# Optimization experiments

Hardware: AMD Instinct MI355X
Metric: run time of the kernel (lower is better)

The kernel has to match this reference:

```python
import jax, jax.numpy as jnp
import numpy as np

N = 131072
N_DIM = 128
NUM_LAYERS = 8
N_MID = NUM_LAYERS - 2  # middle (n_dim -> n_dim) layers


def _sigmoid_layer(h, u_un, w_un, log_a, b):
    # h: [N, in]; u_un: [out, in]; w_un: [out, out]; log_a, b: [out, 1]
    a = jnp.exp(log_a)                      # [out, 1]
    u = jax.nn.softmax(u_un, axis=1)        # row-softmax, matches Softmax(dim=1)
    w = jax.nn.softmax(w_un, axis=1)
    inner = h @ (a * u).T + b[:, 0]         # [N, out]
    return jax.nn.sigmoid(inner) @ w.T      # [N, out]


def setup_inputs() -> dict:
    key = jax.random.key(0)
    ks = jax.random.split(key, 24)
    d = N_DIM
    inp = {
        "x": jax.random.normal(ks[0], (N,), jnp.float32),
        "fy0": jax.random.normal(ks[1], (N,), jnp.float32),
        # first layer (in=2, out=d)
        "u0": jax.random.normal(ks[2], (d, 2), jnp.float32),
        "w0": jax.random.normal(ks[3], (d, d), jnp.float32),
        "la0": jax.random.normal(ks[4], (d, 1), jnp.float32),
        "b0": jax.random.normal(ks[5], (d, 1), jnp.float32),
        # middle layers stacked (in=d, out=d)
        "uM": jax.random.normal(ks[6], (N_MID, d, d), jnp.float32),
        "wM": jax.random.normal(ks[7], (N_MID, d, d), jnp.float32),
        "laM": jax.random.normal(ks[8], (N_MID, d, 1), jnp.float32),
        "bM": jax.random.normal(ks[9], (N_MID, d, 1), jnp.float32),
        # last layer (in=d, out=1)
        "uL": jax.random.normal(ks[10], (1, d), jnp.float32),
        "wL": jax.random.normal(ks[11], (1, 1), jnp.float32),
        "laL": jax.random.normal(ks[12], (1, 1), jnp.float32),
        "bL": jax.random.normal(ks[13], (1, 1), jnp.float32),
        # MLP 1 -> 50 -> 50 -> 1
        "W1": jax.random.normal(ks[14], (50, 1), jnp.float32) * 0.2,
        "b1": jax.random.normal(ks[15], (50,), jnp.float32) * 0.2,
        "W2": jax.random.normal(ks[16], (50, 50), jnp.float32) * 0.1,
        "b2": jax.random.normal(ks[17], (50,), jnp.float32) * 0.1,
        "W3": jax.random.normal(ks[18], (1, 50), jnp.float32) * 0.1,
        "b3": jax.random.normal(ks[19], (1,), jnp.float32) * 0.1,
    }
    return inp


def reference(x, fy0, u0, w0, la0, b0, uM, wM, laM, bM, uL, wL, laL, bL,
              W1, b1, W2, b2, W3, b3):
    # MLP feature net on fy0: [N,1] -> [N,1]
    h = jax.nn.relu(fy0[:, None] @ W1.T + b1)
    h = jax.nn.relu(h @ W2.T + b2)
    theta = h @ W3.T + b3                          # [N, 1]
    mono = jnp.concatenate([x[:, None], theta], 1)  # [N, 2]

    mono = _sigmoid_layer(mono, u0, w0, la0, b0)    # [N, d]

    def step(carry, p):
        u_un, w_un, log_a, b = p
        return _sigmoid_layer(carry, u_un, w_un, log_a, b), None

    mono, _ = jax.lax.scan(step, mono, (uM, wM, laM, bM))
    out = _sigmoid_layer(mono, uL, wL, laL, bL)     # [N, 1]
    return out[:, :, None]                          # [N, 1, 1] matches torch
```

## Files before the change

kernel.cpp:

```cpp
#include <hip/hip_runtime.h>
#include <cstdint>

typedef __attribute__((ext_vector_type(8))) _Float16 half8;
typedef __attribute__((ext_vector_type(2))) _Float16 half2v;
typedef __attribute__((ext_vector_type(16))) float f32x16;
typedef __attribute__((ext_vector_type(4))) float f4;

#define LOG2E 1.44269504088896340f

__device__ __forceinline__ float fast_exp(float x) { return __builtin_amdgcn_exp2f(LOG2E * x); }
__device__ __forceinline__ float sigmoidf(float v) {
    return __builtin_amdgcn_rcpf(1.f + __builtin_amdgcn_exp2f(-LOG2E * v));
}
__device__ __forceinline__ unsigned pk2(float a, float b) {
    half2v h = { (_Float16)a, (_Float16)b };
    return __builtin_bit_cast(unsigned, h);
}
__device__ __forceinline__ void swapl(unsigned& a, unsigned& b) {
    asm volatile("v_permlane32_swap_b32 %0, %1" : "+v"(a), "+v"(b));
}
__device__ __forceinline__ void swaplf(float& a, float& b) {
    asm volatile("v_permlane32_swap_b32 %0, %1" : "+v"(a), "+v"(b));
}
union BU { unsigned u[4]; half8 h; };

constexpr int A0X = 0, A0T = 128, B0O = 256, BMO = 384, VLO = 1152,
              W1P = 1280, B1P = 1344, B2P = 1408, W3P = 1472, ULSF = 1536, CN = 1664;

constexpr int GOFF  = 0;
constexpr int W2HI  = 6 * 65536;
constexpr int W2LO  = W2HI + 8192;
constexpr int CGOFF = W2LO + 8192;
constexpr int WFOFF = CGOFF + 8192;
constexpr int AFOFF = WFOFF + 7 * 65536;

__global__ void prep1_kernel(const float* __restrict__ u0, const float* __restrict__ w0,
                             const float* __restrict__ la0, const float* __restrict__ b0,
                             const float* __restrict__ uM, const float* __restrict__ wM,
                             const float* __restrict__ laM, const float* __restrict__ bM,
                             const float* __restrict__ uL, const float* __restrict__ laL,
                             const float* __restrict__ W1, const float* __restrict__ b1,
                             const float* __restrict__ W2, const float* __restrict__ b2,
                             const float* __restrict__ W3,
                             float* __restrict__ Wf, float* __restrict__ Af,
                             _Float16* __restrict__ W2hi, _Float16* __restrict__ W2lo,
                             float* __restrict__ CgF)
{
    const int b = blockIdx.x, lane = threadIdx.x;
    if (b < 1664) {
        const int m = b >> 7, r = b & 127;
        const float* src;
        float scale = 1.f;
        float* dst;
        if (m == 0) {
            src = w0 + r * 128;
            dst = Wf + r * 128;
        } else if (m & 1) {
            int l = (m - 1) >> 1;
            src = uM + (l * 128 + r) * 128;
            scale = fast_exp(laM[l * 128 + r]);
            dst = Af + l * 16384 + r * 128;
        } else {
            int l = (m - 2) >> 1;
            src = wM + (l * 128 + r) * 128;
            dst = Wf + (l + 1) * 16384 + r * 128;
        }
        float v0 = src[lane], v1 = src[lane + 64];
        float mx = fmaxf(v0, v1);
#pragma unroll
        for (int o = 32; o; o >>= 1) mx = fmaxf(mx, __shfl_xor(mx, o));
        float e0 = fast_exp(v0 - mx), e1 = fast_exp(v1 - mx);
        float ssum = e0 + e1;
#pragma unroll
        for (int o = 32; o; o >>= 1) ssum += __shfl_xor(ssum, o);
        float inv = scale / ssum;
        dst[lane]      = e0 * inv;
        dst[lane + 64] = e1 * inv;
    } else if (b == 1664) {
        for (int j = lane; j < 128; j += 64) {
            float q0 = u0[2 * j], q1 = u0[2 * j + 1];
            float mx = fmaxf(q0, q1);
            float e0 = fast_exp(q0 - mx), e1 = fast_exp(q1 - mx);
            float a = fast_exp(la0[j]) / (e0 + e1);
            CgF[A0X + j] = a * e0;
            CgF[A0T + j] = a * e1;
            CgF[B0O + j] = b0[j];
        }
        CgF[W1P + lane] = (lane < 50) ? W1[lane] : 0.f;
        CgF[B1P + lane] = (lane < 50) ? b1[lane] : 0.f;
        CgF[B2P + lane] = (lane < 50) ? b2[lane] : 0.f;
        CgF[W3P + lane] = (lane < 50) ? W3[lane] : 0.f;
        for (int i = lane; i < 768; i += 64) CgF[BMO + i] = bM[i];
    } else if (b == 1665) {
        float v0 = uL[lane], v1 = uL[lane + 64];
        float mx = fmaxf(v0, v1);
#pragma unroll
        for (int o = 32; o; o >>= 1) mx = fmaxf(mx, __shfl_xor(mx, o));
        float e0 = fast_exp(v0 - mx), e1 = fast_exp(v1 - mx);
        float ssum = e0 + e1;
#pragma unroll
        for (int o = 32; o; o >>= 1) ssum += __shfl_xor(ssum, o);
        float aL = fast_exp(laL[0]) / ssum;
        CgF[ULSF + lane]      = e0 * aL;
        CgF[ULSF + 64 + lane] = e1 * aL;
    } else {
        for (int i = lane; i < 4096; i += 64) {
            int r = i >> 6, c = i & 63;
            float v = (r < 50 && c < 50) ? W2[r * 50 + c] : 0.f;
            _Float16 h = (_Float16)v;
            W2hi[i] = h;
            W2lo[i] = (_Float16)(v - (float)h);
        }
    }
}

__global__ void prep2_kernel(const float* __restrict__ Wf, const float* __restrict__ Af,
                             char* __restrict__ G, float* __restrict__ CgF)
{
    const int b = blockIdx.x, lane = threadIdx.x;
    if (b < 768) {
        const int l = b >> 7, i = b & 127;
        const float* Arow = Af + l * 16384 + i * 128;
        const float* W = Wf + l * 16384;
        float m0 = 0.f, m1 = 0.f;
        for (int k = 0; k < 128; ++k) {
            float a = Arow[k];
            m0 += a * W[k * 128 + lane];
            m1 += a * W[k * 128 + lane + 64];
        }
        char* basehi = G + l * 65536 + i * 256;
        char* baselo = basehi + 32768;
        const int sw = (i & 7) << 4;
        _Float16 h0 = (_Float16)m0, h1 = (_Float16)m1;
        *(_Float16*)(basehi + ((2 * lane) ^ sw))        = h0;
        *(_Float16*)(basehi + ((2 * (lane + 64)) ^ sw)) = h1;
        *(_Float16*)(baselo + ((2 * lane) ^ sw))        = (_Float16)(m0 - (float)h0);
        *(_Float16*)(baselo + ((2 * (lane + 64)) ^ sw)) = (_Float16)(m1 - (float)h1);
    } else {
        const float* W6 = Wf + 6 * 16384;
        float m0 = 0.f, m1 = 0.f;
        for (int i = 0; i < 128; ++i) {
            float u = CgF[ULSF + i];
            m0 += u * W6[i * 128 + lane];
            m1 += u * W6[i * 128 + lane + 64];
        }
        CgF[VLO + lane]      = m0;
        CgF[VLO + 64 + lane] = m1;
    }
}


__device__ __forceinline__ void stage64(char* ls, const char* gs, int tid) {
#pragma unroll
    for (int i = 0; i < 8; ++i)
        __builtin_amdgcn_global_load_lds(
            (const __attribute__((address_space(1))) unsigned*)(uintptr_t)(gs + tid * 16 + i * 8192),
            (__attribute__((address_space(3))) unsigned*)(uintptr_t)(ls + tid * 16 + i * 8192),
            16, 0, 0);
}

__device__ __forceinline__ void epi_nt(const f32x16& a0, const f32x16& a1,
                                       half8& o00, half8& o01, half8& o10, half8& o11,
                                       const float* __restrict__ biasNT, int hi)
{
    f4 bv0 = *(const f4*)(biasNT + 4 * hi);
    f4 bv1 = *(const f4*)(biasNT + 8 + 4 * hi);
    f4 bv2 = *(const f4*)(biasNT + 16 + 4 * hi);
    f4 bv3 = *(const f4*)(biasNT + 24 + 4 * hi);
#pragma unroll
    for (int bt = 0; bt < 2; ++bt) {
        const f32x16& A = bt ? a1 : a0;
        unsigned p00 = pk2(sigmoidf(A[0] + bv0[0]),  sigmoidf(A[1] + bv0[1]));
        unsigned p01 = pk2(sigmoidf(A[2] + bv0[2]),  sigmoidf(A[3] + bv0[3]));
        unsigned p10 = pk2(sigmoidf(A[4] + bv1[0]),  sigmoidf(A[5] + bv1[1]));
        unsigned p11 = pk2(sigmoidf(A[6] + bv1[2]),  sigmoidf(A[7] + bv1[3]));
        unsigned p20 = pk2(sigmoidf(A[8] + bv2[0]),  sigmoidf(A[9] + bv2[1]));
        unsigned p21 = pk2(sigmoidf(A[10] + bv2[2]), sigmoidf(A[11] + bv2[3]));
        unsigned p30 = pk2(sigmoidf(A[12] + bv3[0]), sigmoidf(A[13] + bv3[1]));
        unsigned p31 = pk2(sigmoidf(A[14] + bv3[2]), sigmoidf(A[15] + bv3[3]));
        swapl(p00, p10); swapl(p01, p11);
        swapl(p20, p30); swapl(p21, p31);
        BU u0; u0.u[0] = p00; u0.u[1] = p01; u0.u[2] = p10; u0.u[3] = p11;
        BU u1; u1.u[0] = p20; u1.u[1] = p21; u1.u[2] = p30; u1.u[3] = p31;
        if (bt == 0) { o00 = u0.h; o01 = u1.h; }
        else         { o10 = u0.h; o11 = u1.h; }
    }
}

__device__ __forceinline__ void do_layer(const char* buf,
                                         const half8 (&Bin)[2][8], half8 (&Bout)[2][8],
                                         const float* __restrict__ biasL,
                                         int l31, int hi)
{
    const int sw = (l31 & 7) << 4;
#pragma unroll
    for (int nt = 0; nt < 4; ++nt) {
        f32x16 a0 = {}, a1 = {};
        const char* rhi = buf + (nt * 32 + l31) * 256;
        const char* rlo = rhi + 32768;
#pragma unroll
        for (int ks = 0; ks < 8; ++ks) {
            const int off = (ks * 32 + hi * 16) ^ sw;
            half8 Ah = *(const half8*)(rhi + off);
            half8 Al = *(const half8*)(rlo + off);
            a0 = __builtin_amdgcn_mfma_f32_32x32x16_f16(Ah, Bin[0][ks], a0, 0, 0, 0);
            a1 = __builtin_amdgcn_mfma_f32_32x32x16_f16(Ah, Bin[1][ks], a1, 0, 0, 0);
            a0 = __builtin_amdgcn_mfma_f32_32x32x16_f16(Al, Bin[0][ks], a0, 0, 0, 0);
            a1 = __builtin_amdgcn_mfma_f32_32x32x16_f16(Al, Bin[1][ks], a1, 0, 0, 0);
        }
        epi_nt(a0, a1, Bout[0][2 * nt], Bout[0][2 * nt + 1],
               Bout[1][2 * nt], Bout[1][2 * nt + 1], biasL + 32 * nt, hi);
    }
}

__global__ __launch_bounds__(512, 2)
void mono_main(const float* __restrict__ x, const float* __restrict__ fy0,
               const char* __restrict__ G,
               const _Float16* __restrict__ W2hi, const _Float16* __restrict__ W2lo,
               const float* __restrict__ CgF, const float* __restrict__ b3g,
               const float* __restrict__ bLg, float* __restrict__ out)
{
    extern __shared__ __align__(16) char sm[];
    char* buf0 = sm;
    char* buf1 = sm + 65536;

    const int tid = threadIdx.x;
    const int lane = tid & 63, wave = tid >> 6;
    const int l31 = lane & 31, hi = lane >> 5;
    const int row0 = blockIdx.x * 512 + wave * 64;

    stage64(buf0, G, tid);
    const float b3s = b3g[0], bLs = bLg[0];

    float fy[2] = { fy0[row0 + l31], fy0[row0 + 32 + l31] };
    half8 Bm[2][4];
#pragma unroll
    for (int ks = 0; ks < 4; ++ks) {
        f4 w1a = *(const f4*)(CgF + W1P + 16 * ks + 8 * hi);
        f4 w1b = *(const f4*)(CgF + W1P + 16 * ks + 8 * hi + 4);
        f4 b1a = *(const f4*)(CgF + B1P + 16 * ks + 8 * hi);
        f4 b1b = *(const f4*)(CgF + B1P + 16 * ks + 8 * hi + 4);
#pragma unroll
        for (int bt = 0; bt < 2; ++bt) {
            BU u;
            u.u[0] = pk2(fmaxf(fy[bt] * w1a[0] + b1a[0], 0.f), fmaxf(fy[bt] * w1a[1] + b1a[1], 0.f));
            u.u[1] = pk2(fmaxf(fy[bt] * w1a[2] + b1a[2], 0.f), fmaxf(fy[bt] * w1a[3] + b1a[3], 0.f));
            u.u[2] = pk2(fmaxf(fy[bt] * w1b[0] + b1b[0], 0.f), fmaxf(fy[bt] * w1b[1] + b1b[1], 0.f));
            u.u[3] = pk2(fmaxf(fy[bt] * w1b[2] + b1b[2], 0.f), fmaxf(fy[bt] * w1b[3] + b1b[3], 0.f));
            Bm[bt][ks] = u.h;
        }
    }

    f32x16 a00 = {}, a01 = {}, a10 = {}, a11 = {};
#pragma unroll
    for (int nt = 0; nt < 2; ++nt)
#pragma unroll
        for (int ks = 0; ks < 4; ++ks) {
            half8 Ah = *(const half8*)(W2hi + (nt * 32 + l31) * 64 + ks * 16 + hi * 8);
            half8 Al = *(const half8*)(W2lo + (nt * 32 + l31) * 64 + ks * 16 + hi * 8);
            if (nt == 0) {
                a00 = __builtin_amdgcn_mfma_f32_32x32x16_f16(Ah, Bm[0][ks], a00, 0, 0, 0);
                a10 = __builtin_amdgcn_mfma_f32_32x32x16_f16(Ah, Bm[1][ks], a10, 0, 0, 0);
                a00 = __builtin_amdgcn_mfma_f32_32x32x16_f16(Al, Bm[0][ks], a00, 0, 0, 0);
                a10 = __builtin_amdgcn_mfma_f32_32x32x16_f16(Al, Bm[1][ks], a10, 0, 0, 0);
            } else {
                a01 = __builtin_amdgcn_mfma_f32_32x32x16_f16(Ah, Bm[0][ks], a01, 0, 0, 0);
                a11 = __builtin_amdgcn_mfma_f32_32x32x16_f16(Ah, Bm[1][ks], a11, 0, 0, 0);
                a01 = __builtin_amdgcn_mfma_f32_32x32x16_f16(Al, Bm[0][ks], a01, 0, 0, 0);
                a11 = __builtin_amdgcn_mfma_f32_32x32x16_f16(Al, Bm[1][ks], a11, 0, 0, 0);
            }
        }

    float tp0 = 0.f, tp1 = 0.f;
#pragma unroll
    for (int nt = 0; nt < 2; ++nt)
#pragma unroll
        for (int g = 0; g < 4; ++g) {
            f4 w3 = *(const f4*)(CgF + W3P + 32 * nt + 8 * g + 4 * hi);
            f4 b2v = *(const f4*)(CgF + B2P + 32 * nt + 8 * g + 4 * hi);
            const f32x16& A0 = nt ? a01 : a00;
            const f32x16& A1 = nt ? a11 : a10;
#pragma unroll
            for (int e = 0; e < 4; ++e) {
                tp0 += w3[e] * fmaxf(A0[4 * g + e] + b2v[e], 0.f);
                tp1 += w3[e] * fmaxf(A1[4 * g + e] + b2v[e], 0.f);
            }
        }
    swaplf(tp0, tp1);
    float th = tp0 + tp1 + b3s;
    float t0 = th, t1 = th;
    swaplf(t0, t1);

    float xr[2] = { x[row0 + l31], x[row0 + 32 + l31] };
    float thv[2] = { t0, t1 };
    half8 Bq[2][8], Bp[2][8];
#pragma unroll
    for (int ks = 0; ks < 8; ++ks) {
        f4 axa = *(const f4*)(CgF + A0X + 16 * ks + 8 * hi);
        f4 axb = *(const f4*)(CgF + A0X + 16 * ks + 8 * hi + 4);
        f4 ata = *(const f4*)(CgF + A0T + 16 * ks + 8 * hi);
        f4 atb = *(const f4*)(CgF + A0T + 16 * ks + 8 * hi + 4);
        f4 b0a = *(const f4*)(CgF + B0O + 16 * ks + 8 * hi);
        f4 b0b = *(const f4*)(CgF + B0O + 16 * ks + 8 * hi + 4);
#pragma unroll
        for (int bt = 0; bt < 2; ++bt) {
            BU u;
            u.u[0] = pk2(sigmoidf(axa[0] * xr[bt] + ata[0] * thv[bt] + b0a[0]),
                         sigmoidf(axa[1] * xr[bt] + ata[1] * thv[bt] + b0a[1]));
            u.u[1] = pk2(sigmoidf(axa[2] * xr[bt] + ata[2] * thv[bt] + b0a[2]),
                         sigmoidf(axa[3] * xr[bt] + ata[3] * thv[bt] + b0a[3]));
            u.u[2] = pk2(sigmoidf(axb[0] * xr[bt] + atb[0] * thv[bt] + b0b[0]),
                         sigmoidf(axb[1] * xr[bt] + atb[1] * thv[bt] + b0b[1]));
            u.u[3] = pk2(sigmoidf(axb[2] * xr[bt] + atb[2] * thv[bt] + b0b[2]),
                         sigmoidf(axb[3] * xr[bt] + atb[3] * thv[bt] + b0b[3]));
            Bq[bt][ks] = u.h;
        }
    }
    __syncthreads();

    stage64(buf1, G + 1 * 65536, tid);
    do_layer(buf0, Bq, Bp, CgF + BMO + 0 * 128, l31, hi);
    __syncthreads();
    stage64(buf0, G + 2 * 65536, tid);
    do_layer(buf1, Bp, Bq, CgF + BMO + 1 * 128, l31, hi);
    __syncthreads();
    stage64(buf1, G + 3 * 65536, tid);
    do_layer(buf0, Bq, Bp, CgF + BMO + 2 * 128, l31, hi);
    __syncthreads();
    stage64(buf0, G + 4 * 65536, tid);
    do_layer(buf1, Bp, Bq, CgF + BMO + 3 * 128, l31, hi);
    __syncthreads();
    stage64(buf1, G + 5 * 65536, tid);
    do_layer(buf0, Bq, Bp, CgF + BMO + 4 * 128, l31, hi);
    __syncthreads();
    do_layer(buf1, Bp, Bq, CgF + BMO + 5 * 128, l31, hi);

    float d0 = 0.f, d1 = 0.f;
#pragma unroll
    for (int ks = 0; ks < 8; ++ks) {
        f4 va = *(const f4*)(CgF + VLO + 16 * ks + 8 * hi);
        f4 vb = *(const f4*)(CgF + VLO + 16 * ks + 8 * hi + 4);
        half8 s0 = Bq[0][ks], s1 = Bq[1][ks];
#pragma unroll
        for (int e = 0; e < 4; ++e) {
            d0 += va[e] * (float)s0[e] + vb[e] * (float)s0[e + 4];
            d1 += va[e] * (float)s1[e] + vb[e] * (float)s1[e + 4];
        }
    }
    swaplf(d0, d1);
    out[row0 + lane] = sigmoidf(d0 + d1 + bLs);
}

extern "C" void kernel_launch(void* const* d_in, const int* in_sizes, int n_in,
                              void* d_out, int out_size, void* d_ws, size_t ws_size,
                              hipStream_t stream)
{
    const float* x   = (const float*)d_in[0];
    const float* fy0 = (const float*)d_in[1];
    const float* u0  = (const float*)d_in[2];
    const float* w0  = (const float*)d_in[3];
    const float* la0 = (const float*)d_in[4];
    const float* b0  = (const float*)d_in[5];
    const float* uM  = (const float*)d_in[6];
    const float* wM  = (const float*)d_in[7];
    const float* laM = (const float*)d_in[8];
    const float* bM  = (const float*)d_in[9];
    const float* uL  = (const float*)d_in[10];
    const float* laL = (const float*)d_in[12];
    const float* bL  = (const float*)d_in[13];
    const float* W1  = (const float*)d_in[14];
    const float* b1  = (const float*)d_in[15];
    const float* W2  = (const float*)d_in[16];
    const float* b2  = (const float*)d_in[17];
    const float* W3  = (const float*)d_in[18];
    const float* b3  = (const float*)d_in[19];
    float* out = (float*)d_out;

    char* ws = (char*)d_ws;
    char*     Gz   = ws + GOFF;
    _Float16* W2hi = (_Float16*)(ws + W2HI);
    _Float16* W2lo = (_Float16*)(ws + W2LO);
    float*    CgF  = (float*)(ws + CGOFF);
    float*    Wf   = (float*)(ws + WFOFF);
    float*    Af   = (float*)(ws + AFOFF);

    prep1_kernel<<<1667, 64, 0, stream>>>(u0, w0, la0, b0, uM, wM, laM, bM,
                                          uL, laL, W1, b1, W2, b2, W3,
                                          Wf, Af, W2hi, W2lo, CgF);
    prep2_kernel<<<769, 64, 0, stream>>>(Wf, Af, Gz, CgF);

    static bool attr_set = false;
    if (!attr_set) {
        hipFuncSetAttribute((const void*)mono_main,
                            hipFuncAttributeMaxDynamicSharedMemorySize, 131072);
        attr_set = true;
    }
    mono_main<<<256, 512, 131072, stream>>>(x, fy0, Gz, W2hi, W2lo, CgF, b3, bL, out);
}
```

Baseline: 165.3 us.

## Fuse two weight-prep kernels into one LDS-tiled kernel and fold bias into sigmoid

Replaces the two-stage weight preprocessing (row softmax to global scratch, then a separate matmul kernel) with a single 25-block kernel. Each block computes the softmaxed W into LDS and its slice of A·W directly, which removes one launch and the intermediate global round trip. The middle-layer biases are prescaled by -log2e so each sigmoid in the main kernel becomes a single fma feeding exp2. The cost is fewer, heavier prep blocks with a serial 128-step LDS inner loop, which leaves most of the GPU idle during prep.

```diff
diff --git a/kernel.cpp b/kernel.cpp
--- a/kernel.cpp
+++ b/kernel.cpp
@@ -7,10 +7,14 @@
 typedef __attribute__((ext_vector_type(4))) float f4;
 
 #define LOG2E 1.44269504088896340f
+#define KNL  (-1.44269504088896340f)
 
 __device__ __forceinline__ float fast_exp(float x) { return __builtin_amdgcn_exp2f(LOG2E * x); }
 __device__ __forceinline__ float sigmoidf(float v) {
-    return __builtin_amdgcn_rcpf(1.f + __builtin_amdgcn_exp2f(-LOG2E * v));
+    return __builtin_amdgcn_rcpf(1.f + __builtin_amdgcn_exp2f(KNL * v));
+}
+__device__ __forceinline__ float sigx(float v, float nb) {
+    return __builtin_amdgcn_rcpf(1.f + __builtin_amdgcn_exp2f(fmaf(v, KNL, nb)));
 }
 __device__ __forceinline__ unsigned pk2(float a, float b) {
     half2v h = { (_Float16)a, (_Float16)b };
@@ -25,59 +29,130 @@
 union BU { unsigned u[4]; half8 h; };
 
 constexpr int A0X = 0, A0T = 128, B0O = 256, BMO = 384, VLO = 1152,
-              W1P = 1280, B1P = 1344, B2P = 1408, W3P = 1472, ULSF = 1536, CN = 1664;
+              W1P = 1280, B1P = 1344, B2P = 1408, W3P = 1472, CN = 1536;
 
 constexpr int GOFF  = 0;
 constexpr int W2HI  = 6 * 65536;
 constexpr int W2LO  = W2HI + 8192;
 constexpr int CGOFF = W2LO + 8192;
-constexpr int WFOFF = CGOFF + 8192;
-constexpr int AFOFF = WFOFF + 7 * 65536;
-
-__global__ void prep1_kernel(const float* __restrict__ u0, const float* __restrict__ w0,
-                             const float* __restrict__ la0, const float* __restrict__ b0,
-                             const float* __restrict__ uM, const float* __restrict__ wM,
-                             const float* __restrict__ laM, const float* __restrict__ bM,
-                             const float* __restrict__ uL, const float* __restrict__ laL,
-                             const float* __restrict__ W1, const float* __restrict__ b1,
-                             const float* __restrict__ W2, const float* __restrict__ b2,
-                             const float* __restrict__ W3,
-                             float* __restrict__ Wf, float* __restrict__ Af,
-                             _Float16* __restrict__ W2hi, _Float16* __restrict__ W2lo,
-                             float* __restrict__ CgF)
+
+__global__ __launch_bounds__(256)
+void prep_kernel(const float* __restrict__ u0, const float* __restrict__ w0,
+                 const float* __restrict__ la0, const float* __restrict__ b0,
+                 const float* __restrict__ uM, const float* __restrict__ wM,
+                 const float* __restrict__ laM, const float* __restrict__ bM,
+                 const float* __restrict__ uL, const float* __restrict__ laL,
+                 const float* __restrict__ W1, const float* __restrict__ b1,
+                 const float* __restrict__ W2, const float* __restrict__ b2,
+                 const float* __restrict__ W3,
+                 char* __restrict__ G, _Float16* __restrict__ W2hi,
+                 _Float16* __restrict__ W2lo, float* __restrict__ CgF)
 {
-    const int b = blockIdx.x, lane = threadIdx.x;
-    if (b < 1664) {
-        const int m = b >> 7, r = b & 127;
-        const float* src;
-        float scale = 1.f;
-        float* dst;
-        if (m == 0) {
-            src = w0 + r * 128;
-            dst = Wf + r * 128;
-        } else if (m & 1) {
-            int l = (m - 1) >> 1;
-            src = uM + (l * 128 + r) * 128;
-            scale = fast_exp(laM[l * 128 + r]);
-            dst = Af + l * 16384 + r * 128;
-        } else {
-            int l = (m - 2) >> 1;
-            src = wM + (l * 128 + r) * 128;
-            dst = Wf + (l + 1) * 16384 + r * 128;
-        }
-        float v0 = src[lane], v1 = src[lane + 64];
-        float mx = fmaxf(v0, v1);
-#pragma unroll
-        for (int o = 32; o; o >>= 1) mx = fmaxf(mx, __shfl_xor(mx, o));
-        float e0 = fast_exp(v0 - mx), e1 = fast_exp(v1 - mx);
-        float ssum = e0 + e1;
-#pragma unroll
-        for (int o = 32; o; o >>= 1) ssum += __shfl_xor(ssum, o);
-        float inv = scale / ssum;
-        dst[lane]      = e0 * inv;
-        dst[lane + 64] = e1 * inv;
-    } else if (b == 1664) {
-        for (int j = lane; j < 128; j += 64) {
+    __shared__ float Wl[128 * 136];
+    __shared__ float Al[32 * 132];
+    __shared__ float uls[128];
+
+    const int tid = threadIdx.x, b = blockIdx.x;
+    const bool mblk = (b < 24);
+    const int l = mblk ? (b >> 2) : 6;
+
+    {
+        const float* Wsrc = (l == 0) ? w0 : wM + (l - 1) * 16384;
+        const int r = tid >> 1, h = tid & 1;
+        const float* rp = Wsrc + r * 128 + h * 64;
+        f4 buf[16];
+#pragma unroll
+        for (int v = 0; v < 16; ++v) buf[v] = *(const f4*)(rp + 4 * v);
+        float mx = -1e30f;
+#pragma unroll
+        for (int v = 0; v < 16; ++v)
+#pragma unroll
+            for (int e = 0; e < 4; ++e) mx = fmaxf(mx, buf[v][e]);
+        mx = fmaxf(mx, __shfl_xor(mx, 1));
+        float s = 0.f;
+#pragma unroll
+        for (int v = 0; v < 16; ++v)
+#pragma unroll
+            for (int e = 0; e < 4; ++e) { buf[v][e] = fast_exp(buf[v][e] - mx); s += buf[v][e]; }
+        s += __shfl_xor(s, 1);
+        float inv = 1.f / s;
+#pragma unroll
+        for (int v = 0; v < 16; ++v)
+            *(f4*)(&Wl[r * 136 + h * 64 + 4 * v]) = buf[v] * inv;
+    }
+
+    if (mblk) {
+        const int q = b & 3;
+        const int rl = tid >> 3, part = tid & 7;
+        const int gi = q * 32 + rl;
+        {
+            const float* up = uM + (l * 128 + gi) * 128 + part * 16;
+            f4 ub[4];
+#pragma unroll
+            for (int v = 0; v < 4; ++v) ub[v] = *(const f4*)(up + 4 * v);
+            float mx = -1e30f;
+#pragma unroll
+            for (int v = 0; v < 4; ++v)
+#pragma unroll
+                for (int e = 0; e < 4; ++e) mx = fmaxf(mx, ub[v][e]);
+#pragma unroll
+            for (int o = 1; o < 8; o <<= 1) mx = fmaxf(mx, __shfl_xor(mx, o));
+            float s = 0.f;
+#pragma unroll
+            for (int v = 0; v < 4; ++v)
+#pragma unroll
+                for (int e = 0; e < 4; ++e) { ub[v][e] = fast_exp(ub[v][e] - mx); s += ub[v][e]; }
+#pragma unroll
+            for (int o = 1; o < 8; o <<= 1) s += __shfl_xor(s, o);
+            float sc = fast_exp(laM[l * 128 + gi]) / s;
+#pragma unroll
+            for (int v = 0; v < 4; ++v)
+                *(f4*)(&Al[rl * 132 + part * 16 + 4 * v]) = ub[v] * sc;
+        }
+        __syncthreads();
+        const int j0 = (tid & 7) * 4;
+        f4 acc[4] = {};
+        for (int k = 0; k < 128; ++k) {
+            float a = Al[rl * 132 + k];
+#pragma unroll
+            for (int g = 0; g < 4; ++g)
+                acc[g] += a * *(const f4*)(&Wl[k * 136 + j0 + 32 * g]);
+        }
+        char* basehi = G + l * 65536 + gi * 256;
+        char* baselo = basehi + 32768;
+        const int sw = (gi & 7) << 4;
+#pragma unroll
+        for (int g = 0; g < 4; ++g)
+#pragma unroll
+            for (int e = 0; e < 4; ++e) {
+                const int j = j0 + 32 * g + e;
+                float m = acc[g][e];
+                _Float16 hh = (_Float16)m;
+                *(_Float16*)(basehi + ((2 * j) ^ sw)) = hh;
+                *(_Float16*)(baselo + ((2 * j) ^ sw)) = (_Float16)(m - (float)hh);
+            }
+    } else {
+        if (tid < 64) {
+            float v0 = uL[tid], v1 = uL[tid + 64];
+            float mx = fmaxf(v0, v1);
+#pragma unroll
+            for (int o = 32; o; o >>= 1) mx = fmaxf(mx, __shfl_xor(mx, o));
+            float e0 = fast_exp(v0 - mx), e1 = fast_exp(v1 - mx);
+            float ssum = e0 + e1;
+#pragma unroll
+            for (int o = 32; o; o >>= 1) ssum += __shfl_xor(ssum, o);
+            float aL = fast_exp(laL[0]) / ssum;
+            uls[tid]      = e0 * aL;
+            uls[tid + 64] = e1 * aL;
+        }
+        __syncthreads();
+        if (tid < 128) {
+            float s = 0.f;
+            for (int k = 0; k < 128; ++k) s += uls[k] * Wl[k * 136 + tid];
+            CgF[VLO + tid] = s;
+        }
+        if (tid < 128) {
+            const int j = tid;
             float q0 = u0[2 * j], q1 = u0[2 * j + 1];
             float mx = fmaxf(q0, q1);
             float e0 = fast_exp(q0 - mx), e1 = fast_exp(q1 - mx);
@@ -85,67 +160,21 @@
             CgF[A0X + j] = a * e0;
             CgF[A0T + j] = a * e1;
             CgF[B0O + j] = b0[j];
-        }
-        CgF[W1P + lane] = (lane < 50) ? W1[lane] : 0.f;
-        CgF[B1P + lane] = (lane < 50) ? b1[lane] : 0.f;
-        CgF[B2P + lane] = (lane < 50) ? b2[lane] : 0.f;
-        CgF[W3P + lane] = (lane < 50) ? W3[lane] : 0.f;
-        for (int i = lane; i < 768; i += 64) CgF[BMO + i] = bM[i];
-    } else if (b == 1665) {
-        float v0 = uL[lane], v1 = uL[lane + 64];
-        float mx = fmaxf(v0, v1);
-#pragma unroll
-        for (int o = 32; o; o >>= 1) mx = fmaxf(mx, __shfl_xor(mx, o));
-        float e0 = fast_exp(v0 - mx), e1 = fast_exp(v1 - mx);
-        float ssum = e0 + e1;
-#pragma unroll
-        for (int o = 32; o; o >>= 1) ssum += __shfl_xor(ssum, o);
-        float aL = fast_exp(laL[0]) / ssum;
-        CgF[ULSF + lane]      = e0 * aL;
-        CgF[ULSF + 64 + lane] = e1 * aL;
-    } else {
-        for (int i = lane; i < 4096; i += 64) {
+        } else if (tid < 192) {
+            const int t = tid - 128;
+            CgF[W1P + t] = (t < 50) ? W1[t] : 0.f;
+            CgF[B1P + t] = (t < 50) ? b1[t] : 0.f;
+            CgF[B2P + t] = (t < 50) ? b2[t] : 0.f;
+            CgF[W3P + t] = (t < 50) ? W3[t] : 0.f;
+        }
+        for (int i = tid; i < 768; i += 256) CgF[BMO + i] = KNL * bM[i];
+        for (int i = tid; i < 4096; i += 256) {
             int r = i >> 6, c = i & 63;
             float v = (r < 50 && c < 50) ? W2[r * 50 + c] : 0.f;
             _Float16 h = (_Float16)v;
             W2hi[i] = h;
             W2lo[i] = (_Float16)(v - (float)h);
         }
-    }
-}
-
-__global__ void prep2_kernel(const float* __restrict__ Wf, const float* __restrict__ Af,
-                             char* __restrict__ G, float* __restrict__ CgF)
-{
-    const int b = blockIdx.x, lane = threadIdx.x;
-    if (b < 768) {
-        const int l = b >> 7, i = b & 127;
-        const float* Arow = Af + l * 16384 + i * 128;
-        const float* W = Wf + l * 16384;
-        float m0 = 0.f, m1 = 0.f;
-        for (int k = 0; k < 128; ++k) {
-            float a = Arow[k];
-            m0 += a * W[k * 128 + lane];
-            m1 += a * W[k * 128 + lane + 64];
-        }
-        char* basehi = G + l * 65536 + i * 256;
-        char* baselo = basehi + 32768;
-        const int sw = (i & 7) << 4;
-        _Float16 h0 = (_Float16)m0, h1 = (_Float16)m1;
-        *(_Float16*)(basehi + ((2 * lane) ^ sw))        = h0;
-        *(_Float16*)(basehi + ((2 * (lane + 64)) ^ sw)) = h1;
-        *(_Float16*)(baselo + ((2 * lane) ^ sw))        = (_Float16)(m0 - (float)h0);
-        *(_Float16*)(baselo + ((2 * (lane + 64)) ^ sw)) = (_Float16)(m1 - (float)h1);
-    } else {
-        const float* W6 = Wf + 6 * 16384;
-        float m0 = 0.f, m1 = 0.f;
-        for (int i = 0; i < 128; ++i) {
-            float u = CgF[ULSF + i];
-            m0 += u * W6[i * 128 + lane];
-            m1 += u * W6[i * 128 + lane + 64];
-        }
-        CgF[VLO + lane]      = m0;
-        CgF[VLO + 64 + lane] = m1;
     }
 }
 
@@ -170,14 +199,14 @@
 #pragma unroll
     for (int bt = 0; bt < 2; ++bt) {
         const f32x16& A = bt ? a1 : a0;
-        unsigned p00 = pk2(sigmoidf(A[0] + bv0[0]),  sigmoidf(A[1] + bv0[1]));
-        unsigned p01 = pk2(sigmoidf(A[2] + bv0[2]),  sigmoidf(A[3] + bv0[3]));
-        unsigned p10 = pk2(sigmoidf(A[4] + bv1[0]),  sigmoidf(A[5] + bv1[1]));
-        unsigned p11 = pk2(sigmoidf(A[6] + bv1[2]),  sigmoidf(A[7] + bv1[3]));
-        unsigned p20 = pk2(sigmoidf(A[8] + bv2[0]),  sigmoidf(A[9] + bv2[1]));
-        unsigned p21 = pk2(sigmoidf(A[10] + bv2[2]), sigmoidf(A[11] + bv2[3]));
-        unsigned p30 = pk2(sigmoidf(A[12] + bv3[0]), sigmoidf(A[13] + bv3[1]));
-        unsigned p31 = pk2(sigmoidf(A[14] + bv3[2]), sigmoidf(A[15] + bv3[3]));
+        unsigned p00 = pk2(sigx(A[0], bv0[0]),  sigx(A[1], bv0[1]));
+        unsigned p01 = pk2(sigx(A[2], bv0[2]),  sigx(A[3], bv0[3]));
+        unsigned p10 = pk2(sigx(A[4], bv1[0]),  sigx(A[5], bv1[1]));
+        unsigned p11 = pk2(sigx(A[6], bv1[2]),  sigx(A[7], bv1[3]));
+        unsigned p20 = pk2(sigx(A[8], bv2[0]),  sigx(A[9], bv2[1]));
+        unsigned p21 = pk2(sigx(A[10], bv2[2]), sigx(A[11], bv2[3]));
+        unsigned p30 = pk2(sigx(A[12], bv3[0]), sigx(A[13], bv3[1]));
+        unsigned p31 = pk2(sigx(A[14], bv3[2]), sigx(A[15], bv3[3]));
         swapl(p00, p10); swapl(p01, p11);
         swapl(p20, p30); swapl(p21, p31);
         BU u0; u0.u[0] = p00; u0.u[1] = p01; u0.u[2] = p10; u0.u[3] = p11;
@@ -381,13 +410,10 @@
     _Float16* W2hi = (_Float16*)(ws + W2HI);
     _Float16* W2lo = (_Float16*)(ws + W2LO);
     float*    CgF  = (float*)(ws + CGOFF);
-    float*    Wf   = (float*)(ws + WFOFF);
-    float*    Af   = (float*)(ws + AFOFF);
-
-    prep1_kernel<<<1667, 64, 0, stream>>>(u0, w0, la0, b0, uM, wM, laM, bM,
-                                          uL, laL, W1, b1, W2, b2, W3,
-                                          Wf, Af, W2hi, W2lo, CgF);
-    prep2_kernel<<<769, 64, 0, stream>>>(Wf, Af, Gz, CgF);
+
+    prep_kernel<<<25, 256, 0, stream>>>(u0, w0, la0, b0, uM, wM, laM, bM,
+                                        uL, laL, W1, b1, W2, b2, W3,
+                                        Gz, W2hi, W2lo, CgF);
 
     static bool attr_set = false;
     if (!attr_set) {
```

Result: faster. 154.6 us (-6.5%).
